# Optimization experiments

Hardware: AMD Instinct MI355X
Metric: run time of the kernel (lower is better)

## Reference

```python
import jax, jax.numpy as jnp
import numpy as np

B, N, P, D = 16, 1024, 72, 96
ND, H, K = 64, 4, 16
LN_EPS = 1e-5
ROW_EPS = 1e-8


def topk_sparsify(adj, k):
    # adj: (..., N, N); keep top-k per row (scatter-mask), then row-renormalize
    shp = adj.shape
    n = shp[-1]
    flat = adj.reshape(-1, n)
    _, idx = jax.lax.top_k(flat, k)  # (R, k)
    rows = jnp.arange(flat.shape[0])[:, None]
    mask = jnp.zeros_like(flat).at[rows, idx].set(1.0)
    sp = flat * mask
    sp = sp / (sp.sum(-1, keepdims=True) + ROW_EPS)
    return sp.reshape(shp)


def setup_inputs() -> dict:
    key = jax.random.key(0)
    ks = jax.random.split(key, 12)
    xav1 = np.sqrt(6.0 / (N + ND))  # xavier_uniform bound for (N, ND)
    inp = {
        "patch_features": jax.random.normal(ks[0], (B, N, P, D), jnp.float32),
        "E1": jax.random.uniform(ks[1], (H, N, ND), jnp.float32, -xav1, xav1),
        "E2": jax.random.uniform(ks[2], (H, ND, N), jnp.float32, -xav1, xav1),
        "temperature": jnp.full((H,), 0.5, jnp.float32),
        "fusion_weight": jnp.float32(0.5),
        "dW1": jax.random.normal(ks[3], (D, ND), jnp.float32) / np.sqrt(D),
        "db1": jnp.zeros((ND,), jnp.float32),
        "ln_g": jnp.ones((ND,), jnp.float32),
        "ln_b": jnp.zeros((ND,), jnp.float32),
        "dW2": jax.random.normal(ks[4], (ND, ND), jnp.float32) / np.sqrt(ND),
        "db2": jnp.zeros((ND,), jnp.float32),
        "eW1": jax.random.normal(ks[5], (H, 2 * H), jnp.float32) / np.sqrt(H),
        "eb1": jnp.zeros((2 * H,), jnp.float32),
        "eW2": jax.random.normal(ks[6], (2 * H, 1), jnp.float32) / np.sqrt(2 * H),
        "eb2": jnp.zeros((1,), jnp.float32),
    }
    return inp


def reference(patch_features, E1, E2, temperature, fusion_weight,
              dW1, db1, ln_g, ln_b, dW2, db2, eW1, eb1, eW2, eb2):
    # ---- static multi-head graphs: softmax(relu(E1 @ E2) / T, axis=-1) ----
    s = jax.nn.relu(jnp.einsum('hnd,hdm->hnm', E1, E2))
    static_adjs = jax.nn.softmax(s / temperature[:, None, None], axis=-1)

    # ---- dynamic graphs from mean-pooled patch features ----
    node_repr = patch_features.mean(axis=2)                 # (B, N, D)
    h1 = node_repr @ dW1 + db1                              # (B, N, ND)
    mu = h1.mean(-1, keepdims=True)
    var = ((h1 - mu) ** 2).mean(-1, keepdims=True)
    h1 = (h1 - mu) / jnp.sqrt(var + LN_EPS) * ln_g + ln_b   # LayerNorm
    h1 = jax.nn.relu(h1)                                    # (dropout = identity, eval)
    dyn_emb = h1 @ dW2 + db2                                # (B, N, ND)
    d = jax.nn.relu(jnp.einsum('bnd,hdm->bhnm', dyn_emb, E2))
    dynamic_adjs = jax.nn.softmax(d / temperature[None, :, None, None], axis=-1)

    # ---- top-k sparsify + row renormalize ----
    static_adjs = topk_sparsify(static_adjs, K)             # (H, N, N)
    dynamic_adjs = topk_sparsify(dynamic_adjs, K)           # (B, H, N, N)

    # ---- fuse static + dynamic ----
    fused = (1.0 - fusion_weight) * static_adjs[None] + fusion_weight * dynamic_adjs

    # ---- edge MLP over head dim: (B, N, N, H) -> (B, N, N) ----
    x = jnp.transpose(fused, (0, 2, 3, 1))                  # (B, N, N, H)
    ew = jax.nn.relu(x @ eW1 + eb1) @ eW2 + eb2             # (B, N, N, 1)
    final_adjs = jax.nn.sigmoid(ew[..., 0]) * fused.mean(axis=1)
    return final_adjs, static_adjs, dynamic_adjs
```

## Files before the change

kernel.cpp:

```cpp
#include <hip/hip_runtime.h>

typedef unsigned int u32;
typedef unsigned long long u64;

#define Bn 16
#define Nn 1024
#define Pp 72
#define MARG 3e-4f

#define NEGINF __int_as_float(0xff800000)
#define POSINF __int_as_float(0x7f800000)

#define DPP_STEP(OP, CTRL, RM)                                                 \
  y = __builtin_amdgcn_update_dpp(__float_as_int(v), __float_as_int(v),        \
                                  CTRL, RM, 0xf, false);                       \
  v = OP(v, __int_as_float(y));

#define DPP_RED(NAME, OP)                                                      \
  __device__ __forceinline__ float NAME(float v) {                             \
    int y;                                                                     \
    DPP_STEP(OP, 0x111, 0xf)                                                   \
    DPP_STEP(OP, 0x112, 0xf)                                                   \
    DPP_STEP(OP, 0x114, 0xf)                                                   \
    DPP_STEP(OP, 0x118, 0xf)                                                   \
    DPP_STEP(OP, 0x142, 0xa)                                                   \
    DPP_STEP(OP, 0x143, 0xc)                                                   \
    return __int_as_float(__builtin_amdgcn_readlane(__float_as_int(v), 63));   \
  }

#define FADDOP(a, b) ((a) + (b))
DPP_RED(dmaxf, fmaxf)
DPP_RED(dminf, fminf)
DPP_RED(dsumf, FADDOP)

__device__ __forceinline__ u32 wminu(u32 v) {
#pragma unroll
  for (int off = 1; off < 64; off <<= 1) {
    u32 o = (u32)__shfl_xor((int)v, off, 64);
    v = (o < v) ? o : v;
  }
  return v;
}

template <int MODE>
__device__ __forceinline__ u32 select_row(const float* __restrict__ q,
                                          float* __restrict__ v, int l,
                                          const float* __restrict__ e1row,
                                          const double* __restrict__ edrow,
                                          const float* __restrict__ e2t,
                                          double Td) {
  float lm = q[0];
#pragma unroll
  for (int j = 1; j < 16; ++j) lm = fmaxf(lm, q[j]);
  const float qmax = dmaxf(lm);

  u32 lo = 0u, hi = __float_as_uint(qmax) + 1u;
  u32 kept = 0u;
  bool f16 = false;
  float pvf = 0.0f;
#pragma unroll 1
  while (hi - lo > 1u) {
    u32 mid = (lo + hi) >> 1;
    float pv = __uint_as_float(mid);
    u32 cw = 0;
#pragma unroll
    for (int j = 0; j < 16; ++j)
      cw += (u32)__popcll(__ballot(q[j] >= pv));
    if (cw >= 16u) lo = mid; else hi = mid;
    if (cw == 16u) { f16 = true; pvf = pv; break; }
  }
  float theta, ub;
  if (f16) {
    float vmin = POSINF, umax = -1.0f;
#pragma unroll
    for (int j = 0; j < 16; ++j) {
      if (q[j] >= pvf) { kept |= 1u << j; vmin = fminf(vmin, q[j]); }
      else umax = fmaxf(umax, q[j]);
    }
    theta = dminf(vmin);
    ub = dmaxf(umax);
  } else {
    theta = __uint_as_float(lo);
    u32 cw = 0;
#pragma unroll
    for (int j = 0; j < 16; ++j) {
      cw += (u32)__popcll(__ballot(q[j] > theta));
      if (q[j] > theta) kept |= 1u << j;
    }
    int rr = 16 - (int)cw;
#pragma unroll 1
    for (int it = 0; it < rr; ++it) {
      u32 mc = 0xFFFFFFFFu;
#pragma unroll
      for (int j = 0; j < 16; ++j)
        if (q[j] == theta && !((kept >> j) & 1u)) {
          u32 cc = (u32)((j << 6) | l);
          mc = cc < mc ? cc : mc;
        }
      u32 wm = wminu(mc);
      if ((wm & 63u) == (u32)l) kept |= 1u << (wm >> 6);
    }
    ub = theta;
  }

  if (theta - ub >= MARG) {
    float e[16];
    float es = 0.0f, ek = 0.0f;
#pragma unroll
    for (int j = 0; j < 16; ++j) {
      e[j] = __expf(q[j] - qmax);
      es += e[j];
      if ((kept >> j) & 1u) ek += e[j];
    }
    const float Z = dsumf(es);
    const float EK = dsumf(ek);
    const float inv = 1.0f / (EK + 1e-8f * Z);
#pragma unroll
    for (int j = 0; j < 16; ++j)
      v[j] = ((kept >> j) & 1u) ? (e[j] * inv) : 0.0f;
    return kept;
  } else {
    double qd[16];
    const float thr = ub - MARG;
#pragma unroll 1
    for (int j = 0; j < 16; ++j) {
      if (q[j] >= thr) {
        const int m = l + (j << 6);
        const float* col = e2t + (size_t)m * 64;
        double a = 0.0;
        for (int d = 0; d < 64; ++d) {
          double s = (MODE == 0) ? (double)e1row[d] : edrow[d];
          a = fma(s, (double)col[d], a);
        }
        qd[j] = (a > 0.0 ? a : 0.0) / Td;
      } else {
        qd[j] = (double)q[j];
      }
    }
    double bm = qd[0];
#pragma unroll
    for (int j = 1; j < 16; ++j) bm = qd[j] > bm ? qd[j] : bm;
    float mh = (float)bm;
    float mlo = (float)(bm - (double)mh);
    float whi = dmaxf(mh);
    float wlo = dmaxf(mh == whi ? mlo : NEGINF);
    const double qmaxd = (double)whi + (double)wlo;

    float ev2[16];
    float es2 = 0.0f;
#pragma unroll
    for (int j = 0; j < 16; ++j) { ev2[j] = __expf((float)(qd[j] - qmaxd)); es2 += ev2[j]; }
    const float Z2 = dsumf(es2);

    u32 kept2 = 0;
    float EK2 = 0.0f;
#pragma unroll 1
    for (int it = 0; it < 16; ++it) {
      double bv = -1.0;
      int bjj = -1;
#pragma unroll
      for (int j = 0; j < 16; ++j) {
        bool tk = (((kept2 >> j) & 1u) == 0u) && (qd[j] > bv);
        bv = tk ? qd[j] : bv;
        bjj = tk ? j : bjj;
      }
      float bh = NEGINF, bl = NEGINF;
      if (bjj >= 0) { bh = (float)bv; bl = (float)(bv - (double)bh); }
      float vhi = dmaxf(bh);
      float vlo = dmaxf(bh == vhi ? bl : NEGINF);
      bool elig = (bh == vhi) && (bl == vlo);
      u32 mc = elig ? (u32)((bjj << 6) | l) : 0xFFFFFFFFu;
      u32 mwin = wminu(mc);
      EK2 += __expf((float)(((double)vhi + (double)vlo) - qmaxd));
      if ((mwin & 63u) == (u32)l) kept2 |= 1u << (mwin >> 6);
    }
    const float inv2 = 1.0f / (EK2 + 1e-8f * Z2);
#pragma unroll
    for (int j = 0; j < 16; ++j)
      v[j] = ((kept2 >> j) & 1u) ? (ev2[j] * inv2) : 0.0f;
    return kept2;
  }
}

__device__ __forceinline__ void emit_compact(u32 kept, const float* __restrict__ v,
                                             int l, float* __restrict__ cbase) {
  const u64 lt = ((u64)1 << l) - 1;
  u32 cum = 0;
#pragma unroll
  for (int j = 0; j < 16; ++j) {
    u64 m = __ballot((kept >> j) & 1u);
    u32 idx = cum + (u32)__popcll(m & lt);
    if ((kept >> j) & 1u) {
      cbase[idx] = v[j];
      cbase[16 + idx] = __uint_as_float((u32)(l + (j << 6)));
    }
    cum += (u32)__popcll(m);
  }
}

__global__ __launch_bounds__(256) void k_e2t(const float* __restrict__ E2,
                                             float* __restrict__ E2T) {
  __shared__ float tile[32][65];
  const int h = blockIdx.x >> 5;
  const int m0 = (blockIdx.x & 31) << 5;
  const float* src = E2 + (size_t)h * 65536;
  float* dst = E2T + (size_t)h * 65536;
  const int t = threadIdx.x;
#pragma unroll
  for (int k = 0; k < 8; ++k) {
    int idx = k * 256 + t;
    int d = idx >> 5, mm = idx & 31;
    tile[mm][d] = src[d * 1024 + m0 + mm];
  }
  __syncthreads();
#pragma unroll
  for (int k = 0; k < 8; ++k) {
    int idx = k * 256 + t;
    int mm = idx >> 6, d = idx & 63;
    dst[(size_t)(m0 + mm) * 64 + d] = tile[mm][d];
  }
}

__global__ __launch_bounds__(128) void k_meanmlp(const float* __restrict__ pf,
                                                 const float* __restrict__ dW1,
                                                 const float* __restrict__ db1,
                                                 const float* __restrict__ ln_g,
                                                 const float* __restrict__ ln_b,
                                                 const float* __restrict__ dW2,
                                                 const float* __restrict__ db2,
                                                 double* __restrict__ embD,
                                                 float* __restrict__ embF) {
  __shared__ double ndD[96];
  __shared__ double red[64];
  __shared__ double h1r[64];
  const int t = threadIdx.x;
  const int bn = blockIdx.x;

  if (t < 96) {
    const float* src = pf + (size_t)bn * (Pp * 96) + t;
    double s = 0.0;
    for (int p = 0; p < Pp; ++p) s += (double)src[p * 96];
    ndD[t] = s / 72.0;
  }
  __syncthreads();

  double a = 0.0;
  if (t < 64) {
    a = (double)db1[t];
    for (int d = 0; d < 96; ++d) a = fma(ndD[d], (double)dW1[d * 64 + t], a);
    red[t] = a;
  }
  __syncthreads();
  for (int s2 = 32; s2 >= 1; s2 >>= 1) {
    if (t < s2) red[t] += red[t + s2];
    __syncthreads();
  }
  const double mu = red[0] * (1.0 / 64.0);
  __syncthreads();
  const double dv = a - mu;
  if (t < 64) red[t] = dv * dv;
  __syncthreads();
  for (int s2 = 32; s2 >= 1; s2 >>= 1) {
    if (t < s2) red[t] += red[t + s2];
    __syncthreads();
  }
  const double var = red[0] * (1.0 / 64.0);
  if (t < 64) {
    double xn = dv / sqrt(var + 1e-5) * (double)ln_g[t] + (double)ln_b[t];
    h1r[t] = xn > 0.0 ? xn : 0.0;
  }
  __syncthreads();
  if (t < 64) {
    double e = (double)db2[t];
    for (int k = 0; k < 64; ++k) e = fma(h1r[k], (double)dW2[k * 64 + t], e);
    embD[(size_t)bn * 64 + t] = e;
    embF[(size_t)bn * 64 + t] = (float)e;
  }
}

template <int MODE>
__global__ __launch_bounds__(256) void k_dot(const float* __restrict__ e1f,
                                             const float* __restrict__ embF,
                                             const float* __restrict__ E2,
                                             const float* __restrict__ temp,
                                             float* __restrict__ outp) {
  __shared__ float embsh[64][16];
  const int t = threadIdx.x;
  const int r0 = blockIdx.x * 16;
  int h;
  size_t erow;
  if (MODE == 0) {
    h = r0 >> 10;
    erow = (size_t)r0;
  } else {
    int b = r0 >> 12;
    h = (r0 >> 10) & 3;
    int n0 = r0 & 1023;
    erow = (size_t)(b << 10) + n0;
  }
  const float* efa = (MODE == 0) ? (e1f + erow * 64) : (embF + erow * 64);
  const float* e2 = E2 + (size_t)h * 65536;
  const float invT = 1.0f / temp[h];

#pragma unroll
  for (int i = t; i < 1024; i += 256) {
    int g = i & 15, d = i >> 4;
    embsh[d][g] = efa[g * 64 + d];
  }
  __syncthreads();

  const int s = t >> 7;
  const int c1 = (t & 127) * 4;
  const int c2 = c1 + 512;

  float acc[8][8];
#pragma unroll
  for (int g = 0; g < 8; ++g)
#pragma unroll
    for (int x = 0; x < 8; ++x) acc[g][x] = 0.0f;

#pragma unroll 4
  for (int d = 0; d < 64; ++d) {
    float4 va = *(const float4*)(e2 + d * 1024 + c1);
    float4 vb = *(const float4*)(e2 + d * 1024 + c2);
    float4 ea = *(const float4*)&embsh[d][8 * s];
    float4 eb = *(const float4*)&embsh[d][8 * s + 4];
    float sg;
#define ROWFMA(g, SS)                                                          \
    sg = SS;                                                                   \
    acc[g][0] = fmaf(sg, va.x, acc[g][0]);                                     \
    acc[g][1] = fmaf(sg, va.y, acc[g][1]);                                     \
    acc[g][2] = fmaf(sg, va.z, acc[g][2]);                                     \
    acc[g][3] = fmaf(sg, va.w, acc[g][3]);                                     \
    acc[g][4] = fmaf(sg, vb.x, acc[g][4]);                                     \
    acc[g][5] = fmaf(sg, vb.y, acc[g][5]);                                     \
    acc[g][6] = fmaf(sg, vb.z, acc[g][6]);                                     \
    acc[g][7] = fmaf(sg, vb.w, acc[g][7]);
    ROWFMA(0, ea.x) ROWFMA(1, ea.y) ROWFMA(2, ea.z) ROWFMA(3, ea.w)
    ROWFMA(4, eb.x) ROWFMA(5, eb.y) ROWFMA(6, eb.z) ROWFMA(7, eb.w)
#undef ROWFMA
  }

#pragma unroll
  for (int g = 0; g < 8; ++g) {
    float* orow = outp + (size_t)(r0 + 8 * s + g) * 1024;
    float4 o1, o2;
    o1.x = fmaxf(acc[g][0], 0.0f) * invT;
    o1.y = fmaxf(acc[g][1], 0.0f) * invT;
    o1.z = fmaxf(acc[g][2], 0.0f) * invT;
    o1.w = fmaxf(acc[g][3], 0.0f) * invT;
    o2.x = fmaxf(acc[g][4], 0.0f) * invT;
    o2.y = fmaxf(acc[g][5], 0.0f) * invT;
    o2.z = fmaxf(acc[g][6], 0.0f) * invT;
    o2.w = fmaxf(acc[g][7], 0.0f) * invT;
    *(float4*)(orow + c1) = o1;
    *(float4*)(orow + c2) = o2;
  }
}

template <int MODE>
__global__ __launch_bounds__(256) void k_selc(const float* __restrict__ e1f,
                                              const double* __restrict__ embD,
                                              const float* __restrict__ E2T,
                                              const float* __restrict__ temp,
                                              float* __restrict__ outp,
                                              float* __restrict__ cmp) {
  const int t = threadIdx.x;
  const int w = t >> 6, l = t & 63;
  const int r = blockIdx.x * 4 + w;
  int h;
  size_t erow;
  if (MODE == 0) {
    h = r >> 10;
    erow = (size_t)r;
  } else {
    int b = r >> 12;
    h = (r >> 10) & 3;
    int n = r & 1023;
    erow = (size_t)(b << 10) + n;
  }
  const float* e2t = E2T + (size_t)h * 65536;
  const double Td = (double)temp[h];
  float* row = outp + (size_t)r * 1024;

  float q[16], v[16];
#pragma unroll
  for (int j = 0; j < 16; ++j) q[j] = row[l + (j << 6)];

  u32 kept = select_row<MODE>(q, v, l,
                              (MODE == 0) ? (e1f + erow * 64) : nullptr,
                              (MODE == 1) ? (embD + erow * 64) : nullptr,
                              e2t, Td);
#pragma unroll
  for (int j = 0; j < 16; ++j) row[l + (j << 6)] = v[j];
  emit_compact(kept, v, l, cmp + (size_t)r * 32);
}

__global__ __launch_bounds__(256) void k_fusec(const float* __restrict__ cmpd,
                                               const float* __restrict__ cmp0,
                                               float* __restrict__ fin,
                                               const float* __restrict__ eW1,
                                               const float* __restrict__ eb1,
                                               const float* __restrict__ eW2,
                                               const float* __restrict__ eb2,
                                               const float* __restrict__ fwp) {
  __shared__ float fused[4][1024];
  const int t = threadIdx.x;
  const int bn = blockIdx.x;
  const int b = bn >> 10, n = bn & 1023;
  const float fw = fwp[0];
  const float w1 = 1.0f - fw;

  float4* fz = (float4*)&fused[0][0];
  float4 z; z.x = 0.f; z.y = 0.f; z.z = 0.f; z.w = 0.f;
#pragma unroll
  for (int k = 0; k < 4; ++k) fz[t + 256 * k] = z;
  __syncthreads();

  if (t < 64) {
    int h = t >> 4, k = t & 15;
    const float* cb = cmp0 + ((size_t)(h * 1024 + n)) * 32;
    float val = cb[k];
    int col = (int)__float_as_uint(cb[16 + k]);
    fused[h][col] = w1 * val;
  }
  __syncthreads();
  if (t < 64) {
    int h = t >> 4, k = t & 15;
    const float* cb = cmpd + ((size_t)((b * 4 + h) * 1024 + n)) * 32;
    float val = cb[k];
    int col = (int)__float_as_uint(cb[16 + k]);
    fused[h][col] += fw * val;
  }
  __syncthreads();

  float W1[4][8], B1v[8], W2v[8];
#pragma unroll
  for (int hh = 0; hh < 4; ++hh)
#pragma unroll
    for (int j = 0; j < 8; ++j) W1[hh][j] = eW1[hh * 8 + j];
#pragma unroll
  for (int j = 0; j < 8; ++j) { B1v[j] = eb1[j]; W2v[j] = eW2[j]; }
  const float b2 = eb2[0];

  float* orow = fin + (size_t)bn * 1024;
#pragma unroll
  for (int k = 0; k < 4; ++k) {
    const int col = t + 256 * k;
    const float f0 = fused[0][col];
    const float f1 = fused[1][col];
    const float f2 = fused[2][col];
    const float f3 = fused[3][col];
    float ew = b2;
#pragma unroll
    for (int j = 0; j < 8; ++j) {
      float hj = B1v[j];
      hj = fmaf(f0, W1[0][j], hj);
      hj = fmaf(f1, W1[1][j], hj);
      hj = fmaf(f2, W1[2][j], hj);
      hj = fmaf(f3, W1[3][j], hj);
      ew = fmaf(fmaxf(hj, 0.0f), W2v[j], ew);
    }
    const float mean = (f0 + f1 + f2 + f3) * 0.25f;
    const float sg = 1.0f / (1.0f + __expf(-ew));
    orow[col] = sg * mean;
  }
}

extern "C" void kernel_launch(void* const* d_in, const int* in_sizes, int n_in,
                              void* d_out, int out_size, void* d_ws, size_t ws_size,
                              hipStream_t stream) {
  const float* pf   = (const float*)d_in[0];
  const float* E1   = (const float*)d_in[1];
  const float* E2   = (const float*)d_in[2];
  const float* temp = (const float*)d_in[3];
  const float* fw   = (const float*)d_in[4];
  const float* dW1  = (const float*)d_in[5];
  const float* db1  = (const float*)d_in[6];
  const float* ln_g = (const float*)d_in[7];
  const float* ln_b = (const float*)d_in[8];
  const float* dW2  = (const float*)d_in[9];
  const float* db2  = (const float*)d_in[10];
  const float* eW1  = (const float*)d_in[11];
  const float* eb1  = (const float*)d_in[12];
  const float* eW2  = (const float*)d_in[13];
  const float* eb2  = (const float*)d_in[14];

  float* out_final = (float*)d_out;
  float* out_stat  = out_final + (size_t)Bn * Nn * Nn;
  float* out_dyn   = out_stat + (size_t)4 * Nn * Nn;

  char* wsb = (char*)d_ws;
  double* embD = (double*)wsb;
  float* embF  = (float*)(wsb + (8u << 20));
  float* E2T   = (float*)(wsb + (12u << 20));
  float* cmp0  = (float*)(wsb + (13u << 20));
  float* cmpd  = (float*)(wsb + (14u << 20));

  k_e2t<<<128, 256, 0, stream>>>(E2, E2T);
  k_meanmlp<<<Bn * Nn, 128, 0, stream>>>(pf, dW1, db1, ln_g, ln_b, dW2, db2, embD, embF);
  k_dot<0><<<256, 256, 0, stream>>>(E1, nullptr, E2, temp, out_stat);
  k_selc<0><<<1024, 256, 0, stream>>>(E1, nullptr, E2T, temp, out_stat, cmp0);
  k_dot<1><<<4096, 256, 0, stream>>>(nullptr, embF, E2, temp, out_dyn);
  k_selc<1><<<16384, 256, 0, stream>>>(nullptr, embD, E2T, temp, out_dyn, cmpd);
  k_fusec<<<16384, 256, 0, stream>>>(cmpd, cmp0, out_final, eW1, eb1, eW2, eb2, fw);
}
```

Baseline: 574.4 us.

## Fuse logit dot product and top-k selection into one kernel via LDS

Merges the dot-product kernel and the per-row top-k selection kernel. The ReLU/temperature-scaled logits for 16 rows are staged in a 64 KB shared-memory tile instead of being written to global memory and read back. Each wave then selects and normalizes four rows in sequence and writes the sparse rows and compact outputs. This removes a full global read of the dense logit tensor and one launch per mode. In exchange, the large LDS footprint and fewer workgroups reduce occupancy during the selection phase.

```diff
diff --git a/kernel.cpp b/kernel.cpp
--- a/kernel.cpp
+++ b/kernel.cpp
@@ -279,12 +279,16 @@
 }
 
 template <int MODE>
-__global__ __launch_bounds__(256) void k_dot(const float* __restrict__ e1f,
-                                             const float* __restrict__ embF,
-                                             const float* __restrict__ E2,
-                                             const float* __restrict__ temp,
-                                             float* __restrict__ outp) {
+__global__ __launch_bounds__(256) void k_dotsel(const float* __restrict__ e1f,
+                                                const float* __restrict__ embF,
+                                                const double* __restrict__ embD,
+                                                const float* __restrict__ E2,
+                                                const float* __restrict__ E2T,
+                                                const float* __restrict__ temp,
+                                                float* __restrict__ outp,
+                                                float* __restrict__ cmp) {
   __shared__ float embsh[64][16];
+  __shared__ float lgs[16][1024];
   const int t = threadIdx.x;
   const int r0 = blockIdx.x * 16;
   int h;
@@ -300,7 +304,9 @@
   }
   const float* efa = (MODE == 0) ? (e1f + erow * 64) : (embF + erow * 64);
   const float* e2 = E2 + (size_t)h * 65536;
+  const float* e2t = E2T + (size_t)h * 65536;
   const float invT = 1.0f / temp[h];
+  const double Td = (double)temp[h];
 
 #pragma unroll
   for (int i = t; i < 1024; i += 256) {
@@ -343,7 +349,6 @@
 
 #pragma unroll
   for (int g = 0; g < 8; ++g) {
-    float* orow = outp + (size_t)(r0 + 8 * s + g) * 1024;
     float4 o1, o2;
     o1.x = fmaxf(acc[g][0], 0.0f) * invT;
     o1.y = fmaxf(acc[g][1], 0.0f) * invT;
@@ -353,47 +358,27 @@
     o2.y = fmaxf(acc[g][5], 0.0f) * invT;
     o2.z = fmaxf(acc[g][6], 0.0f) * invT;
     o2.w = fmaxf(acc[g][7], 0.0f) * invT;
-    *(float4*)(orow + c1) = o1;
-    *(float4*)(orow + c2) = o2;
-  }
-}
-
-template <int MODE>
-__global__ __launch_bounds__(256) void k_selc(const float* __restrict__ e1f,
-                                              const double* __restrict__ embD,
-                                              const float* __restrict__ E2T,
-                                              const float* __restrict__ temp,
-                                              float* __restrict__ outp,
-                                              float* __restrict__ cmp) {
-  const int t = threadIdx.x;
+    *(float4*)&lgs[8 * s + g][c1] = o1;
+    *(float4*)&lgs[8 * s + g][c2] = o2;
+  }
+  __syncthreads();
+
   const int w = t >> 6, l = t & 63;
-  const int r = blockIdx.x * 4 + w;
-  int h;
-  size_t erow;
-  if (MODE == 0) {
-    h = r >> 10;
-    erow = (size_t)r;
-  } else {
-    int b = r >> 12;
-    h = (r >> 10) & 3;
-    int n = r & 1023;
-    erow = (size_t)(b << 10) + n;
-  }
-  const float* e2t = E2T + (size_t)h * 65536;
-  const double Td = (double)temp[h];
-  float* row = outp + (size_t)r * 1024;
-
-  float q[16], v[16];
-#pragma unroll
-  for (int j = 0; j < 16; ++j) q[j] = row[l + (j << 6)];
-
-  u32 kept = select_row<MODE>(q, v, l,
-                              (MODE == 0) ? (e1f + erow * 64) : nullptr,
-                              (MODE == 1) ? (embD + erow * 64) : nullptr,
-                              e2t, Td);
-#pragma unroll
-  for (int j = 0; j < 16; ++j) row[l + (j << 6)] = v[j];
-  emit_compact(kept, v, l, cmp + (size_t)r * 32);
+#pragma unroll 1
+  for (int i2 = 0; i2 < 4; ++i2) {
+    const int rloc = w * 4 + i2;
+    const size_t r = (size_t)r0 + rloc;
+    float q[16], v[16];
+#pragma unroll
+    for (int j = 0; j < 16; ++j) q[j] = lgs[rloc][l + (j << 6)];
+    u32 kept = select_row<MODE>(
+        q, v, l, (MODE == 0) ? (e1f + r * 64) : nullptr,
+        (MODE == 1) ? (embD + (erow + rloc) * 64) : nullptr, e2t, Td);
+    float* row = outp + r * 1024;
+#pragma unroll
+    for (int j = 0; j < 16; ++j) row[l + (j << 6)] = v[j];
+    emit_compact(kept, v, l, cmp + r * 32);
+  }
 }
 
 __global__ __launch_bounds__(256) void k_fusec(const float* __restrict__ cmpd,
@@ -499,9 +484,7 @@
 
   k_e2t<<<128, 256, 0, stream>>>(E2, E2T);
   k_meanmlp<<<Bn * Nn, 128, 0, stream>>>(pf, dW1, db1, ln_g, ln_b, dW2, db2, embD, embF);
-  k_dot<0><<<256, 256, 0, stream>>>(E1, nullptr, E2, temp, out_stat);
-  k_selc<0><<<1024, 256, 0, stream>>>(E1, nullptr, E2T, temp, out_stat, cmp0);
-  k_dot<1><<<4096, 256, 0, stream>>>(nullptr, embF, E2, temp, out_dyn);
-  k_selc<1><<<16384, 256, 0, stream>>>(nullptr, embD, E2T, temp, out_dyn, cmpd);
+  k_dotsel<0><<<256, 256, 0, stream>>>(E1, nullptr, nullptr, E2, E2T, temp, out_stat, cmp0);
+  k_dotsel<1><<<4096, 256, 0, stream>>>(nullptr, embF, embD, E2, E2T, temp, out_dyn, cmpd);
   k_fusec<<<16384, 256, 0, stream>>>(cmpd, cmp0, out_final, eW1, eb1, eW2, eb2, fw);
 }
```

Result: slower. 688.8 us (+19.9%).
